# Optimization experiments

Measured on AMD Instinct MI355X. Metric: run time of the kernel, lower is better.

Reference implementation:

```python
import jax, jax.numpy as jnp
from jax import lax
import numpy as np

DN = ('NCHW', 'OIHW', 'NCHW')

def _conv(x, w, b, s):
    # torch Conv2d(kernel=3, padding=1, stride=s)
    y = lax.conv_general_dilated(x, w, (s, s), ((1, 1), (1, 1)), dimension_numbers=DN)
    return y + b[None, :, None, None]

def _convT(x, w, b, s):
    # torch ConvTranspose2d weight layout [in, out, kh, kw]; kernel=3, padding=1, output_padding=s-1
    wk = jnp.flip(w, (2, 3)).transpose(1, 0, 2, 3)  # -> OIHW
    y = lax.conv_general_dilated(x, wk, (1, 1), ((1, s), (1, s)), lhs_dilation=(s, s), dimension_numbers=DN)
    return y + b[None, :, None, None]

def _inorm(x, eps=1e-5):
    # torch InstanceNorm2d (affine=False)
    m = jnp.mean(x, (2, 3), keepdims=True)
    v = jnp.var(x, (2, 3), keepdims=True)
    return (x - m) * lax.rsqrt(v + eps)

def _prelu(x, a):
    return jnp.where(x >= 0, x, a * x)

def _block(x, w, b, a, s):
    return _prelu(_inorm(_conv(x, w, b, s)), a)

def _sage(x, src, tgt, wl, bl, wr, n):
    # PyG SAGEConv, mean aggregation: lin_l(scatter_mean(x[src] -> tgt)) + lin_r(x)
    deg = jnp.zeros((n,), x.dtype).at[tgt].add(1.0)
    agg = jnp.zeros((x.shape[0], n, x.shape[2]), x.dtype).at[:, tgt].add(x[:, src])
    agg = agg / jnp.maximum(deg, 1.0)[None, :, None]
    return jnp.einsum('bnc,oc->bno', agg, wl) + bl + jnp.einsum('bnc,oc->bno', x, wr)

def setup_inputs() -> dict:
    keys = iter(jax.random.split(jax.random.key(0), 64))
    def rn(shape, s=0.05):
        return jax.random.normal(next(keys), shape, jnp.float32) * s
    inp = {}
    inp['x'] = jax.random.normal(next(keys), (16, 1, 400, 400), jnp.float32)
    inp['edges'] = jax.random.randint(next(keys), (2, 5000), 0, 625, jnp.int32)
    for name, (ci, co) in zip(['d4', 'd3', 'd2', 'd1'], [(1, 32), (32, 64), (64, 128), (128, 256)]):
        inp['w_' + name] = rn((co, ci, 3, 3)); inp['b_' + name] = rn((co,))
        inp['a_' + name] = jnp.full((1,), 0.25, jnp.float32)
    inp['w_bot'] = rn((256, 256, 3, 3)); inp['b_bot'] = rn((256,))
    inp['a_bot'] = jnp.full((1,), 0.25, jnp.float32)
    for i in ['1', '2']:
        inp['wl' + i] = rn((256, 256)); inp['bl' + i] = rn((256,)); inp['wr' + i] = rn((256, 256))
    for name, (ci, co) in zip(['u1', 'u2', 'u3'], [(512, 128), (256, 64), (128, 32)]):
        inp['w_' + name] = rn((ci, co, 3, 3)); inp['b_' + name] = rn((co,))
        inp['a_' + name] = jnp.full((1,), 0.25, jnp.float32)
    inp['w_u4'] = rn((64, 2, 3, 3)); inp['b_u4'] = rn((2,))
    return inp

def reference(x, edges, w_d4, b_d4, a_d4, w_d3, b_d3, a_d3, w_d2, b_d2, a_d2, w_d1, b_d1, a_d1, w_bot, b_bot, a_bot, wl1, bl1, wr1, wl2, bl2, wr2, w_u1, b_u1, a_u1, w_u2, b_u2, a_u2, w_u3, b_u3, a_u3, w_u4, b_u4):
    xs = []
    x = _block(x, w_d4, b_d4, a_d4, 2); xs.append(x)   # [B,32,200,200]
    x = _block(x, w_d3, b_d3, a_d3, 2); xs.append(x)   # [B,64,100,100]
    x = _block(x, w_d2, b_d2, a_d2, 2); xs.append(x)   # [B,128,50,50]
    x = _block(x, w_d1, b_d1, a_d1, 2); xs.append(x)   # [B,256,25,25]
    x = _block(x, w_bot, b_bot, a_bot, 1)              # [B,256,25,25]
    B = x.shape[0]
    x = x.reshape(B, 256, -1).transpose(0, 2, 1)       # [B,625,256]
    src, tgt = edges[0], edges[1]
    x = jax.nn.relu(_sage(x, src, tgt, wl1, bl1, wr1, 625))
    x = jax.nn.relu(_sage(x, src, tgt, wl2, bl2, wr2, 625))
    x = x.transpose(0, 2, 1).reshape(B, 256, 25, 25)
    x = jnp.concatenate([xs[3], x], 1)                 # 512 ch
    x = _prelu(_inorm(_convT(x, w_u1, b_u1, 2)), a_u1) # [B,128,50,50]
    x = jnp.concatenate([xs[2], x], 1)
    x = _prelu(_inorm(_convT(x, w_u2, b_u2, 2)), a_u2) # [B,64,100,100]
    x = jnp.concatenate([xs[1], x], 1)
    x = _prelu(_inorm(_convT(x, w_u3, b_u3, 2)), a_u3) # [B,32,200,200]
    x = jnp.concatenate([xs[0], x], 1)
    return _convT(x, w_u4, b_u4, 2)                    # [B,2,400,400], conv_only top
```

## Files before the change

### kernel.cpp

```cpp
#include <hip/hip_runtime.h>
#include <hip/hip_bf16.h>

typedef __hip_bfloat16 bf16;

typedef __bf16 bf16x8 __attribute__((ext_vector_type(8)));
typedef float  f32x16 __attribute__((ext_vector_type(16)));

static __device__ __forceinline__ float bf(const bf16 v){ return __bfloat162float(v); }
static __device__ __forceinline__ float bfu(unsigned short u){
  unsigned fw = ((unsigned)u) << 16; float v; __builtin_memcpy(&v, &fw, 4); return v;
}

static __device__ __forceinline__ float ldm(const void* p, long i, int f){
  return f ? ((const float*)p)[i] : __bfloat162float(((const bf16*)p)[i]);
}
static __device__ __forceinline__ void stm(void* p, long i, int f, float v){
  if(f) ((float*)p)[i] = v; else ((bf16*)p)[i] = __float2bfloat16(v);
}
static __device__ __forceinline__ unsigned short bfbits(float v){
  __hip_bfloat16 h = __float2bfloat16(v);
  return *(unsigned short*)&h;
}

__global__ void k_detect(const void* __restrict__ w, int* __restrict__ mode){
  if(blockIdx.x == 0 && threadIdx.x == 0){
    const unsigned int* u = (const unsigned int*)w;
    int saneLo = 0;
    for(int i = 0; i < 64; i++){
      unsigned short lo = (unsigned short)(u[i] & 0xFFFFu);
      unsigned int fw = ((unsigned int)lo) << 16;
      float v; __builtin_memcpy(&v, &fw, 4);
      float a = fabsf(v);
      if(a > 1e-7f && a < 100.f) saneLo++;
    }
    *mode = (saneLo >= 48) ? 0 : 1;
  }
}

__global__ void k_wtrans(const void* __restrict__ w, float* __restrict__ wT,
                         const int* __restrict__ dmode, int C){
  int idx = blockIdx.x * 256 + threadIdx.x;
  if(idx >= C * C) return;
  int dm = *dmode;
  int o = idx % C, c = idx / C;
  wT[idx] = ldm(w, (long)o * C + c, dm);
}

__global__ void k_wtrans4(const void* __restrict__ w, bf16* __restrict__ wF,
                          const int* __restrict__ dmode, int Cin, int Cout){
  int idx = blockIdx.x * 256 + threadIdx.x;
  if(idx >= Cin * Cout * 9) return;
  int dm = *dmode;
  int e = idx & 7;
  int L = (idx >> 3) & 63;
  int r = idx >> 9;
  int NC = Cout >> 5;
  int nc = r % NC; r /= NC;
  int t  = r % 9;
  int kc = r / 9;
  int ci = kc*16 + (L>>5)*8 + e;
  int co = nc*32 + (L&31);
  wF[idx] = __float2bfloat16(ldm(w, ((long)ci*Cout + co)*9 + t, dm));
}

__global__ void k_wtrans5(const void* __restrict__ w, bf16* __restrict__ wF,
                          const int* __restrict__ dmode, int Cin, int Cout){
  int idx = blockIdx.x * 256 + threadIdx.x;
  if(idx >= Cin * Cout * 9) return;
  int dm = *dmode;
  int e = idx & 7;
  int L = (idx >> 3) & 63;
  int r = idx >> 9;
  int NC = Cout >> 5;
  int nc = r % NC; r /= NC;
  int t  = r % 9;
  int kc = r / 9;
  int ci = kc*16 + (L>>5)*8 + e;
  int co = nc*32 + (L&31);
  wF[idx] = __float2bfloat16(ldm(w, ((long)co*Cin + ci)*9 + t, dm));
}

__global__ __launch_bounds__(256, 4)
void k_conv_d4(const void* __restrict__ in, long in_off,
               const void* __restrict__ w, const void* __restrict__ bias,
               bf16* __restrict__ out, const int* __restrict__ dmode)
{
  __shared__ float sW[288];
  __shared__ float sB[32];
  int tid = threadIdx.x;
  int dm = *dmode;
  for(int e = tid; e < 288; e += 256) sW[e] = ldm(w, e, dm);
  if(tid < 32)  sB[tid] = ldm(bias, tid, dm);
  __syncthreads();
  int r = tid / 50, jt = tid % 50;
  if(r >= 5) return;
  int ho = blockIdx.x * 5 + r;
  int b  = blockIdx.z;
  int j0 = jt * 4;

  float x[3][9];
  long ibase = in_off + (long)b * 160000;
  #pragma unroll
  for(int rr = 0; rr < 3; rr++){
    int ir = 2*ho - 1 + rr;
    if(ir < 0 || ir >= 400){
      #pragma unroll
      for(int c = 0; c < 9; c++) x[rr][c] = 0.f;
      continue;
    }
    long rb = ibase + (long)ir * 400;
    int c0 = 2*j0 - 1;
    #pragma unroll
    for(int c = 0; c < 9; c++){
      int ic = c0 + c;
      x[rr][c] = (ic >= 0 && ic < 400) ? ldm(in, rb + ic, dm) : 0.f;
    }
  }

  long obase = ((long)b * 32) * 40000 + (long)ho * 200 + j0;
  for(int co = 0; co < 32; co++){
    const float* wv = &sW[co*9];
    float bv = sB[co];
    float a[4];
    #pragma unroll
    for(int p = 0; p < 4; p++){
      float s = bv;
      #pragma unroll
      for(int kh = 0; kh < 3; kh++)
        #pragma unroll
        for(int kw = 0; kw < 3; kw++)
          s += x[kh][2*p + kw] * wv[kh*3 + kw];
      a[p] = s;
    }
    ushort4 pk;
    pk.x = bfbits(a[0]); pk.y = bfbits(a[1]); pk.z = bfbits(a[2]); pk.w = bfbits(a[3]);
    *(ushort4*)&out[obase + (long)co * 40000] = pk;
  }
}

template<int CW, int NWC, int NWM, int S, int OCC>
__global__ __launch_bounds__(256, OCC)
void k_convSM(const void* __restrict__ in, long in_off, int fin_sel,
              const bf16* __restrict__ wF, const void* __restrict__ bias,
              void* __restrict__ out, int fout,
              const int* __restrict__ dmode,
              int Cin, int Hin, int Win, int Cout, int Hout, int Wout, int nym)
{
  constexpr int CP = 40;
  constexpr int HALF = CW/2;
  __shared__ unsigned short sX[3*CW*CP];
  int tid  = threadIdx.x;
  int lane = tid & 63;
  int wv   = tid >> 6;
  int nc   = wv % NWC;
  int mt   = wv / NWC;
  int ho   = blockIdx.x;
  int colg = blockIdx.y % nym;
  int cog  = blockIdx.y / nym;
  int b    = blockIdx.z;
  int dm   = *dmode;
  int fin  = (fin_sel == 2) ? dm : fin_sel;
  int NCtot = Cout >> 5;
  int chunk = cog*NWC + nc;
  int jl   = mt*32 + (lane & 31);
  int hi   = lane >> 5;
  int C0   = S*(colg*NWM*32);
  int ir0  = S*ho - 1;

  f32x16 acc;
  #pragma unroll
  for(int q = 0; q < 16; q++) acc[q] = 0.f;

  int p0, p1, p2;
  if(S == 2){ p0 = jl; p1 = HALF + jl; p2 = jl + 1; }
  else      { p0 = jl; p1 = jl + 1;    p2 = jl + 2; }

  for(int ci0 = 0; ci0 < Cin; ci0 += 32){
    for(int e = tid; e < 12*CW; e += 256){
      int c  = e % CW;
      int s  = e / CW;
      int kg = s & 3, r = s >> 2;
      int ir = ir0 + r;
      int ic = C0 - 1 + c;
      unsigned pk0, pk1, pk2, pk3;
      if(ir >= 0 && ir < Hin && ic >= 0 && ic < Win){
        long step = (long)Hin*Win;
        long base = in_off + ((long)b*Cin + ci0 + kg*8)*step + (long)ir*Win + ic;
        unsigned short t8[8];
        #pragma unroll
        for(int u = 0; u < 8; u++) t8[u] = bfbits(ldm(in, base + u*step, fin));
        pk0 = t8[0] | ((unsigned)t8[1]<<16);
        pk1 = t8[2] | ((unsigned)t8[3]<<16);
        pk2 = t8[4] | ((unsigned)t8[5]<<16);
        pk3 = t8[6] | ((unsigned)t8[7]<<16);
      } else { pk0=0; pk1=0; pk2=0; pk3=0; }
      int pos = (S == 2) ? ((c&1) ? HALF + (c>>1) : (c>>1)) : c;
      uint4 q; q.x=pk0; q.y=pk1; q.z=pk2; q.w=pk3;
      *(uint4*)&sX[(r*CW + pos)*CP + kg*8] = q;
    }
    __syncthreads();

    #pragma unroll
    for(int kg2 = 0; kg2 < 2; kg2++){
      int kbase = 8*hi + kg2*16;
      bf16x8 x[9];
      #pragma unroll
      for(int r = 0; r < 3; r++){
        x[r*3+0] = *(const bf16x8*)&sX[(r*CW + p0)*CP + kbase];
        x[r*3+1] = *(const bf16x8*)&sX[(r*CW + p1)*CP + kbase];
        x[r*3+2] = *(const bf16x8*)&sX[(r*CW + p2)*CP + kbase];
      }
      int kc = (ci0 >> 4) + kg2;
      const bf16x8* wb = ((const bf16x8*)wF) + ((long)(kc*9)*NCtot + chunk)*64 + lane;
      const long ws = (long)NCtot*64;
      #pragma unroll
      for(int t = 0; t < 9; t++){
        bf16x8 w = wb[(long)t*ws];
        acc = __builtin_amdgcn_mfma_f32_32x32x16_bf16(w, x[t], acc, 0,0,0);
      }
    }
    __syncthreads();
  }

  int j = colg*NWM*32 + jl;
  if(j < Wout){
    #pragma unroll
    for(int r16 = 0; r16 < 16; r16++){
      int co = chunk*32 + (r16&3) + 8*(r16>>2) + 4*hi;
      float bv = ldm(bias, co, dm);
      stm(out, ((long)b*Cout + co)*Hout*Wout + (long)ho*Wout + j, fout, acc[r16] + bv);
    }
  }
}

__global__ void k_inorm_prelu(void* __restrict__ x, int f, int HW,
                              const void* __restrict__ a, const int* __restrict__ dmode)
{
  int dm = *dmode;
  long base = (long)blockIdx.x * HW;
  float s = 0.f, s2 = 0.f;
  int vec = (f == 0) && ((HW & 3) == 0);
  if(vec){
    const ushort4* vp = (const ushort4*)((const bf16*)x + base);
    int n = HW >> 2;
    for(int i = threadIdx.x; i < n; i += 256){
      ushort4 v = vp[i];
      float a0 = bfu(v.x), a1 = bfu(v.y), a2 = bfu(v.z), a3 = bfu(v.w);
      s  += (a0 + a1) + (a2 + a3);
      s2 += (a0*a0 + a1*a1) + (a2*a2 + a3*a3);
    }
  } else {
    for(int i = threadIdx.x; i < HW; i += 256){ float v = ldm(x, base + i, f); s += v; s2 += v*v; }
  }
  __shared__ float sh[256], sh2[256];
  sh[threadIdx.x] = s; sh2[threadIdx.x] = s2; __syncthreads();
  for(int off = 128; off > 0; off >>= 1){
    if(threadIdx.x < off){ sh[threadIdx.x] += sh[threadIdx.x+off]; sh2[threadIdx.x] += sh2[threadIdx.x+off]; }
    __syncthreads();
  }
  float mean = sh[0] / HW;
  float var  = sh2[0] / HW - mean * mean;
  float inv  = rsqrtf(fmaxf(var, 0.f) + 1e-5f);
  float alpha = ldm(a, 0, dm);
  if(vec){
    ushort4* vp = (ushort4*)((bf16*)x + base);
    int n = HW >> 2;
    for(int i = threadIdx.x; i < n; i += 256){
      ushort4 v = vp[i];
      float t[4] = { bfu(v.x), bfu(v.y), bfu(v.z), bfu(v.w) };
      #pragma unroll
      for(int k = 0; k < 4; k++){
        float u = (t[k] - mean) * inv;
        t[k] = u >= 0.f ? u : alpha * u;
      }
      ushort4 o;
      o.x = bfbits(t[0]); o.y = bfbits(t[1]); o.z = bfbits(t[2]); o.w = bfbits(t[3]);
      vp[i] = o;
    }
  } else {
    for(int i = threadIdx.x; i < HW; i += 256){
      float v = (ldm(x, base + i, f) - mean) * inv;
      stm(x, base + i, f, v >= 0.f ? v : alpha * v);
    }
  }
}

__global__ void k_transpose(const float* __restrict__ in, float* __restrict__ out, int B, int C, int N){
  long idx = (long)blockIdx.x * 256 + threadIdx.x;
  long total = (long)B * C * N; if(idx >= total) return;
  int c = (int)(idx % C); long t = idx / C; int n = (int)(t % N); int b = (int)(t / N);
  out[idx] = in[((long)b * C + c) * N + n];
}

__global__ void k_deg(const int* __restrict__ tgt, float* __restrict__ deg, int E){
  int e = blockIdx.x * 256 + threadIdx.x;
  if(e < E) atomicAdd(&deg[tgt[e]], 1.0f);
}

__global__ void k_scatter(const float* __restrict__ xT, const int* __restrict__ src,
                          const int* __restrict__ tgt, float* __restrict__ agg,
                          int E, int C, int N, int B)
{
  int t = blockIdx.x * 256 + threadIdx.x;
  if(t >= E * C) return;
  int c = t % C; int e = t / C;
  int s = src[e], d = tgt[e];
  for(int b = 0; b < B; b++){
    atomicAdd(&agg[((long)b * N + d) * C + c], xT[((long)b * N + s) * C + c]);
  }
}

#define TN 5
__global__ void k_sage2(const float* __restrict__ xT, const float* __restrict__ agg,
                        const float* __restrict__ deg,
                        const float* __restrict__ wlT, const float* __restrict__ wrT,
                        const void* __restrict__ bl,
                        float* __restrict__ out, const int* __restrict__ dmode,
                        int B, int N, int C, int transpose_out)
{
  int o  = threadIdx.x;
  int n0 = blockIdx.x * TN;
  int b  = blockIdx.y;
  __shared__ float sX[TN][256];
  __shared__ float sA[TN][256];
  #pragma unroll
  for(int j = 0; j < TN; j++){
    int n = n0 + j;
    float dinv = 1.0f / fmaxf(deg[n], 1.0f);
    long base = ((long)b * N + n) * C;
    sX[j][o] = xT[base + o];
    sA[j][o] = agg[base + o] * dinv;
  }
  __syncthreads();
  int dm = *dmode;
  float bv = ldm(bl, o, dm);
  float acc[TN];
  #pragma unroll
  for(int j = 0; j < TN; j++) acc[j] = bv;
  #pragma unroll 4
  for(int c = 0; c < 256; c++){
    float wlv = wlT[(long)c * 256 + o];
    float wrv = wrT[(long)c * 256 + o];
    #pragma unroll
    for(int j = 0; j < TN; j++){
      acc[j] += sA[j][c] * wlv + sX[j][c] * wrv;
    }
  }
  #pragma unroll
  for(int j = 0; j < TN; j++){
    int n = n0 + j;
    float v = fmaxf(acc[j], 0.f);
    if(transpose_out) out[((long)b * C + o) * N + n] = v;
    else              out[((long)b * N + n) * C + o] = v;
  }
}

template<int CW, int NWC, int NWM, int OCC>
__global__ __launch_bounds__(256, OCC)
void k_convTM(const void* __restrict__ inA, int fA, int C1,
              const void* __restrict__ inB, int fB, int C2,
              const bf16* __restrict__ wF, const void* __restrict__ bias,
              bf16* __restrict__ out, const int* __restrict__ dmode,
              int Hin, int Win, int Cout)
{
  constexpr int CP = 40;
  __shared__ unsigned short sX[2*CW*CP];
  int tid  = threadIdx.x;
  int lane = tid & 63;
  int wv   = tid >> 6;
  int nc   = wv % NWC;
  int mt   = wv / NWC;
  int j0   = mt * 32;
  int i    = blockIdx.x;
  int b    = blockIdx.z;
  int dm   = *dmode;
  int Cin  = C1 + C2;
  int ln   = lane & 31;
  int hi   = lane >> 5;

  f32x16 acc0, acc1, acc2, acc3;
  #pragma unroll
  for(int q = 0; q < 16; q++){ acc0[q]=0.f; acc1[q]=0.f; acc2[q]=0.f; acc3[q]=0.f; }

  int xoff = (j0 + ln)*CP + 8*hi;

  for(int ci0 = 0; ci0 < Cin; ci0 += 32){
    for(int e = tid; e < 8*CW; e += 256){
      int col = e % CW;
      int s   = e / CW;
      int kg  = s & 3, row = s >> 2;
      int ii  = i + row;
      unsigned pk0, pk1, pk2, pk3;
      if(ii < Hin && col < Win){
        int cib = ci0 + kg*8;
        const void* sp; int ff; long base; long step = (long)Hin*Win;
        if(cib < C1){ sp = inA; ff = fA; base = ((long)b*C1 + cib)*step + (long)ii*Win + col; }
        else        { sp = inB; ff = fB; base = ((long)b*C2 + (cib-C1))*step + (long)ii*Win + col; }
        unsigned short t8[8];
        #pragma unroll
        for(int u = 0; u < 8; u++) t8[u] = bfbits(ldm(sp, base + u*step, ff));
        pk0 = t8[0] | ((unsigned)t8[1]<<16);
        pk1 = t8[2] | ((unsigned)t8[3]<<16);
        pk2 = t8[4] | ((unsigned)t8[5]<<16);
        pk3 = t8[6] | ((unsigned)t8[7]<<16);
      } else { pk0=0; pk1=0; pk2=0; pk3=0; }
      uint4 q; q.x=pk0; q.y=pk1; q.z=pk2; q.w=pk3;
      *(uint4*)&sX[(row*CW + col)*CP + kg*8] = q;
    }
    __syncthreads();

    #pragma unroll
    for(int kg2 = 0; kg2 < 2; kg2++){
      int base = xoff + kg2*16;
      bf16x8 x00 = *(const bf16x8*)&sX[base];
      bf16x8 x01 = *(const bf16x8*)&sX[base + CP];
      bf16x8 x10 = *(const bf16x8*)&sX[base + CW*CP];
      bf16x8 x11 = *(const bf16x8*)&sX[base + CW*CP + CP];
      int kc = (ci0 >> 4) + kg2;
      const bf16x8* wb = ((const bf16x8*)wF) + ((long)(kc*9)*NWC + nc)*64 + lane;
      const int ws = NWC*64;
      bf16x8 w0=wb[0],    w1=wb[ws],   w2=wb[2*ws], w3=wb[3*ws], w4=wb[4*ws],
             w5=wb[5*ws], w6=wb[6*ws], w7=wb[7*ws], w8=wb[8*ws];
      acc0 = __builtin_amdgcn_mfma_f32_32x32x16_bf16(w4, x00, acc0, 0,0,0);
      acc1 = __builtin_amdgcn_mfma_f32_32x32x16_bf16(w5, x00, acc1, 0,0,0);
      acc1 = __builtin_amdgcn_mfma_f32_32x32x16_bf16(w3, x01, acc1, 0,0,0);
      acc2 = __builtin_amdgcn_mfma_f32_32x32x16_bf16(w7, x00, acc2, 0,0,0);
      acc2 = __builtin_amdgcn_mfma_f32_32x32x16_bf16(w1, x10, acc2, 0,0,0);
      acc3 = __builtin_amdgcn_mfma_f32_32x32x16_bf16(w8, x00, acc3, 0,0,0);
      acc3 = __builtin_amdgcn_mfma_f32_32x32x16_bf16(w6, x01, acc3, 0,0,0);
      acc3 = __builtin_amdgcn_mfma_f32_32x32x16_bf16(w2, x10, acc3, 0,0,0);
      acc3 = __builtin_amdgcn_mfma_f32_32x32x16_bf16(w0, x11, acc3, 0,0,0);
    }
    __syncthreads();
  }

  int j = j0 + ln;
  if(j < Win){
    int Wout = 2*Win;
    #pragma unroll
    for(int r = 0; r < 16; r++){
      int co = nc*32 + (r&3) + 8*(r>>2) + 4*hi;
      float bv = ldm(bias, co, dm);
      long base0 = (((long)b*Cout + co)*2*Hin + 2*i)*(long)Wout + 2*j;
      unsigned p0 = bfbits(acc0[r]+bv) | ((unsigned)bfbits(acc1[r]+bv) << 16);
      unsigned p1 = bfbits(acc2[r]+bv) | ((unsigned)bfbits(acc3[r]+bv) << 16);
      *(unsigned*)&out[base0]        = p0;
      *(unsigned*)&out[base0 + Wout] = p1;
    }
  }
}

__global__ __launch_bounds__(256, 2)
void k_convT8(const bf16* __restrict__ inA, const bf16* __restrict__ inB,
              const void* __restrict__ w, const void* __restrict__ bias,
              void* __restrict__ out, long out_off, int fout_sel,
              const int* __restrict__ dmode, int Hin, int Win)
{
  __shared__ float sW[64*2*9];
  __shared__ float sB[2];
  int tid = threadIdx.x;
  int dm = *dmode;
  for(int e = tid; e < 64*2*9; e += 256) sW[e] = ldm(w, e, dm);
  if(tid < 2) sB[tid] = ldm(bias, tid, dm);
  __syncthreads();
  int r  = tid / 50;
  int jt = tid % 50;
  if(r >= 5) return;
  int i  = blockIdx.x * 5 + r;
  int b  = blockIdx.z;
  int j0 = jt * 4;
  int fout = (fout_sel == 2) ? dm : fout_sel;

  float acc[2][4][4];
  #pragma unroll
  for(int co = 0; co < 2; co++)
    #pragma unroll
    for(int p = 0; p < 4; p++){
      acc[co][p][0]=0.f; acc[co][p][1]=0.f; acc[co][p][2]=0.f; acc[co][p][3]=0.f;
    }

  bool e4   = (j0 + 4 < Win);
  bool row1 = (i + 1 < Hin);

  for(int ci = 0; ci < 64; ci++){
    const bf16* src = (ci < 32) ? inA : inB;
    int cc = ci & 31;
    const bf16* rp = src + ((long)b*32 + cc)*(long)Hin*Win + (long)i*Win + j0;
    float x0[5], x1[5];
    ushort4 v0 = *(const ushort4*)rp;
    x0[0]=bfu(v0.x); x0[1]=bfu(v0.y); x0[2]=bfu(v0.z); x0[3]=bfu(v0.w);
    x0[4] = e4 ? bf(rp[4]) : 0.f;
    if(row1){
      ushort4 v1 = *(const ushort4*)(rp + Win);
      x1[0]=bfu(v1.x); x1[1]=bfu(v1.y); x1[2]=bfu(v1.z); x1[3]=bfu(v1.w);
      x1[4] = e4 ? bf(rp[Win + 4]) : 0.f;
    } else {
      x1[0]=0.f; x1[1]=0.f; x1[2]=0.f; x1[3]=0.f; x1[4]=0.f;
    }
    const float* wp = &sW[ci*18];
    float wv[18];
    #pragma unroll
    for(int k = 0; k < 18; k++) wv[k] = wp[k];
    #pragma unroll
    for(int p = 0; p < 4; p++){
      float a00 = x0[p], a01 = x0[p+1], a10 = x1[p], a11 = x1[p+1];
      #pragma unroll
      for(int co = 0; co < 2; co++){
        const float* wc = &wv[co*9];
        acc[co][p][0] += a00*wc[4];
        acc[co][p][1] += a00*wc[5] + a01*wc[3];
        acc[co][p][2] += a00*wc[7] + a10*wc[1];
        acc[co][p][3] += a00*wc[8] + a01*wc[6] + a10*wc[2] + a11*wc[0];
      }
    }
  }
  int Wout = 2*Win;
  #pragma unroll
  for(int co = 0; co < 2; co++){
    float bv = sB[co];
    long base = out_off + (((long)b*2 + co)*2*Hin + 2*i)*(long)Wout + 2*j0;
    #pragma unroll
    for(int p = 0; p < 4; p++){
      stm(out, base + 2*p,            fout, acc[co][p][0] + bv);
      stm(out, base + 2*p + 1,        fout, acc[co][p][1] + bv);
      stm(out, base + 2*p + Wout,     fout, acc[co][p][2] + bv);
      stm(out, base + 2*p + Wout + 1, fout, acc[co][p][3] + bv);
    }
  }
}

static inline int cdiv(long a, long b){ return (int)((a + b - 1) / b); }

extern "C" void kernel_launch(void* const* d_in, const int* in_sizes, int n_in,
                              void* d_out, int out_size, void* d_ws, size_t ws_size,
                              hipStream_t stream) {
  const void* x_in  = d_in[0];
  const int*  edges = (const int*)d_in[1];
  const int* src = edges;
  const int* tgt = edges + 5000;
  const void *w_d4=d_in[2],  *b_d4=d_in[3],  *a_d4=d_in[4];
  const void *w_d3=d_in[5],  *b_d3=d_in[6],  *a_d3=d_in[7];
  const void *w_d2=d_in[8],  *b_d2=d_in[9],  *a_d2=d_in[10];
  const void *w_d1=d_in[11], *b_d1=d_in[12], *a_d1=d_in[13];
  const void *w_bot=d_in[14],*b_bot=d_in[15],*a_bot=d_in[16];
  const void *wl1=d_in[17], *bl1=d_in[18], *wr1=d_in[19];
  const void *wl2=d_in[20], *bl2=d_in[21], *wr2=d_in[22];
  const void *w_u1=d_in[23], *b_u1=d_in[24], *a_u1=d_in[25];
  const void *w_u2=d_in[26], *b_u2=d_in[27], *a_u2=d_in[28];
  const void *w_u3=d_in[29], *b_u3=d_in[30], *a_u3=d_in[31];
  const void *w_u4=d_in[32], *b_u4=d_in[33];

  const int NNODE = 625, E = 5000, CG = 256;

  const long TAIL = 4096 + 4*262144L + (589824L + 147456L + 36864L) * 2;
  const long ENCW = 976896L * 2;
  int Bc = 16;
  while(Bc > 1 && (7680000L * Bc + TAIL) > (long)ws_size) Bc >>= 1;
  int enc_in_pool = (Bc >= 8);
  if(!enc_in_pool){
    Bc = 16;
    while(Bc > 1 && (7680000L * Bc + TAIL + ENCW) > (long)ws_size) Bc >>= 1;
  }

  char* wsb = (char*)d_ws;
  long o_xs1  = 2560000L * Bc;
  long o_BIGA = 3840000L * Bc;
  long o_BIGB = 6400000L * Bc;
  long o_deg  = 7680000L * Bc;
  bf16*  xs0 = (bf16*)wsb;
  bf16*  xs1 = (bf16*)(wsb + o_xs1);
  bf16*  xs2 = (bf16*)(wsb + o_BIGA);
  bf16*  xs3 = (bf16*)(wsb + o_BIGA +  640000L*Bc);
  float* bot = (float*)(wsb + o_BIGA +  960000L*Bc);
  float* xT  = (float*)(wsb + o_BIGA + 1600000L*Bc);
  bf16*  u1  = (bf16*)(wsb + o_BIGA + 1600000L*Bc);
  bf16*  u3  = (bf16*)(wsb + o_BIGA);
  float* agg = (float*)(wsb + o_BIGB);
  float* g1  = (float*)(wsb + o_BIGB +  640000L*Bc);
  bf16*  u2  = (bf16*)(wsb + o_BIGB);
  float* deg = (float*)(wsb + o_deg);
  int*  mode = (int*)(wsb + o_deg + 3072);
  float* wlT1 = (float*)(wsb + o_deg + 4096);
  float* wrT1 = wlT1 + 65536;
  float* wlT2 = wrT1 + 65536;
  float* wrT2 = wlT2 + 65536;
  bf16*  wTu1 = (bf16*)(wrT2 + 65536);
  bf16*  wTu2 = wTu1 + 589824;
  bf16*  wTu3 = wTu2 + 147456;
  bf16*  wTd3 = enc_in_pool ? (bf16*)(wsb + o_BIGA + 2240000L*Bc) : (wTu3 + 36864);
  bf16*  wTd2 = wTd3 + 18432;
  bf16*  wTd1 = wTd2 + 73728;
  bf16*  wTdB = wTd1 + 294912;
  float* g2  = bot;

  hipLaunchKernelGGL(k_detect, dim3(1), dim3(1), 0, stream, w_d4, mode);

  hipMemsetAsync(deg, 0, NNODE*sizeof(float), stream);
  hipLaunchKernelGGL(k_deg, dim3(cdiv(E,256)), dim3(256), 0, stream, tgt, deg, E);
  hipLaunchKernelGGL(k_wtrans, dim3(256), dim3(256), 0, stream, wl1, wlT1, mode, CG);
  hipLaunchKernelGGL(k_wtrans, dim3(256), dim3(256), 0, stream, wr1, wrT1, mode, CG);
  hipLaunchKernelGGL(k_wtrans, dim3(256), dim3(256), 0, stream, wl2, wlT2, mode, CG);
  hipLaunchKernelGGL(k_wtrans, dim3(256), dim3(256), 0, stream, wr2, wrT2, mode, CG);
  hipLaunchKernelGGL(k_wtrans4, dim3(cdiv(589824,256)), dim3(256), 0, stream, w_u1, wTu1, mode, 512, 128);
  hipLaunchKernelGGL(k_wtrans4, dim3(cdiv(147456,256)), dim3(256), 0, stream, w_u2, wTu2, mode, 256, 64);
  hipLaunchKernelGGL(k_wtrans4, dim3(cdiv(36864,256)),  dim3(256), 0, stream, w_u3, wTu3, mode, 128, 32);

  for(int bo = 0; bo < 16; bo += Bc){
    long x_off   = (long)bo * 160000;
    long out_off = (long)bo * 320000;

    hipLaunchKernelGGL(k_wtrans5, dim3(cdiv(18432,256)),  dim3(256), 0, stream, w_d3, wTd3, mode, 32, 64);
    hipLaunchKernelGGL(k_wtrans5, dim3(cdiv(73728,256)),  dim3(256), 0, stream, w_d2, wTd2, mode, 64, 128);
    hipLaunchKernelGGL(k_wtrans5, dim3(cdiv(294912,256)), dim3(256), 0, stream, w_d1, wTd1, mode, 128, 256);
    hipLaunchKernelGGL(k_wtrans5, dim3(cdiv(589824,256)), dim3(256), 0, stream, w_bot, wTdB, mode, 256, 256);

    hipLaunchKernelGGL(k_conv_d4, dim3(40, 1, Bc), dim3(256), 0, stream,
                       x_in, x_off, w_d4, b_d4, xs0, mode);
    hipLaunchKernelGGL(k_inorm_prelu, dim3(Bc*32), dim3(256), 0, stream, xs0, 0, 40000, a_d4, mode);
    hipLaunchKernelGGL((k_convSM<130,2,2,2,4>), dim3(100, 2, Bc), dim3(256), 0, stream,
                       xs0, 0L, 0, wTd3, b_d3, xs1, 0, mode, 32, 200, 200, 64, 100, 100, 2);
    hipLaunchKernelGGL(k_inorm_prelu, dim3(Bc*64), dim3(256), 0, stream, xs1, 0, 10000, a_d3, mode);
    hipLaunchKernelGGL((k_convSM<66,4,1,2,4>), dim3(50, 2, Bc), dim3(256), 0, stream,
                       xs1, 0L, 0, wTd2, b_d2, xs2, 0, mode, 64, 100, 100, 128, 50, 50, 2);
    hipLaunchKernelGGL(k_inorm_prelu, dim3(Bc*128), dim3(256), 0, stream, xs2, 0, 2500, a_d2, mode);
    hipLaunchKernelGGL((k_convSM<66,4,1,2,4>), dim3(25, 2, Bc), dim3(256), 0, stream,
                       xs2, 0L, 0, wTd1, b_d1, xs3, 0, mode, 128, 50, 50, 256, 25, 25, 1);
    hipLaunchKernelGGL(k_inorm_prelu, dim3(Bc*256), dim3(256), 0, stream, xs3, 0, 625, a_d1, mode);
    hipLaunchKernelGGL((k_convSM<34,4,1,1,4>), dim3(25, 2, Bc), dim3(256), 0, stream,
                       xs3, 0L, 0, wTdB, b_bot, bot, 1, mode, 256, 25, 25, 256, 25, 25, 1);
    hipLaunchKernelGGL(k_inorm_prelu, dim3(Bc*256), dim3(256), 0, stream, bot, 1, 625, a_bot, mode);

    { long n = (long)Bc*CG*NNODE;
      hipLaunchKernelGGL(k_transpose, dim3(cdiv(n,256)), dim3(256), 0, stream, bot, xT, Bc, CG, NNODE); }
    hipMemsetAsync(agg, 0, 640000L*Bc, stream);
    hipLaunchKernelGGL(k_scatter, dim3(cdiv((long)E*CG,256)), dim3(256), 0, stream, xT, src, tgt, agg, E, CG, NNODE, Bc);
    hipLaunchKernelGGL(k_sage2, dim3(125, Bc), dim3(256), 0, stream,
                       xT, agg, deg, wlT1, wrT1, bl1, g1, mode, Bc, NNODE, CG, 0);
    hipMemsetAsync(agg, 0, 640000L*Bc, stream);
    hipLaunchKernelGGL(k_scatter, dim3(cdiv((long)E*CG,256)), dim3(256), 0, stream, g1, src, tgt, agg, E, CG, NNODE, Bc);
    hipLaunchKernelGGL(k_sage2, dim3(125, Bc), dim3(256), 0, stream,
                       g1, agg, deg, wlT2, wrT2, bl2, g2, mode, Bc, NNODE, CG, 1);

    hipLaunchKernelGGL((k_convTM<34,4,1,4>), dim3(25, 1, Bc), dim3(256), 0, stream,
                       xs3, 0, 256, g2, 1, 256, wTu1, b_u1, u1, mode, 25, 25, 128);
    hipLaunchKernelGGL(k_inorm_prelu, dim3(Bc*128), dim3(256), 0, stream, u1, 0, 2500, a_u1, mode);
    hipLaunchKernelGGL((k_convTM<66,2,2,4>), dim3(50, 1, Bc), dim3(256), 0, stream,
                       xs2, 0, 128, u1, 0, 128, wTu2, b_u2, u2, mode, 50, 50, 64);
    hipLaunchKernelGGL(k_inorm_prelu, dim3(Bc*64), dim3(256), 0, stream, u2, 0, 10000, a_u2, mode);
    hipLaunchKernelGGL((k_convTM<130,1,4,4>), dim3(100, 1, Bc), dim3(256), 0, stream,
                       xs1, 0, 64, u2, 0, 64, wTu3, b_u3, u3, mode, 100, 100, 32);
    hipLaunchKernelGGL(k_inorm_prelu, dim3(Bc*32), dim3(256), 0, stream, u3, 0, 40000, a_u3, mode);
    hipLaunchKernelGGL(k_convT8, dim3(40, 1, Bc), dim3(256), 0, stream,
                       xs0, u3, w_u4, b_u4, d_out, out_off, 2, mode, 200, 200);
  }
}
```

Measured before the change: 980.1 us.

## Run SAGE linear layers on bf16 MFMA with pre-swizzled weights

Replaces the scalar FP32 SAGE dense kernel with an MFMA 32x32x16 bf16 kernel. Node rows (x and degree-normalised aggregate) are staged to LDS as bf16, and the weights are pre-packed into the MFMA fragment layout by a new transpose kernel. The output is written either transposed or through an LDS-staged coalesced store. This cuts the FP32 FMA cost of the two 256x256 linear layers but lowers input and weight precision to bf16.

```diff
diff --git a/kernel.cpp b/kernel.cpp
--- a/kernel.cpp
+++ b/kernel.cpp
@@ -37,13 +37,19 @@
   }
 }
 
-__global__ void k_wtrans(const void* __restrict__ w, float* __restrict__ wT,
-                         const int* __restrict__ dmode, int C){
+__global__ void k_wtrans6(const void* __restrict__ w, bf16* __restrict__ wF,
+                          const int* __restrict__ dmode){
   int idx = blockIdx.x * 256 + threadIdx.x;
-  if(idx >= C * C) return;
+  if(idx >= 65536) return;
   int dm = *dmode;
-  int o = idx % C, c = idx / C;
-  wT[idx] = ldm(w, (long)o * C + c, dm);
+  int e = idx & 7;
+  int L = (idx >> 3) & 63;
+  int r = idx >> 9;
+  int nc = r & 7;
+  int kc = r >> 3;
+  int o = nc*32 + (L & 31);
+  int c = kc*16 + (L >> 5)*8 + e;
+  wF[idx] = __float2bfloat16(ldm(w, (long)o*256 + c, dm));
 }
 
 __global__ void k_wtrans4(const void* __restrict__ w, bf16* __restrict__ wF,
@@ -310,48 +316,89 @@
   }
 }
 
-#define TN 5
-__global__ void k_sage2(const float* __restrict__ xT, const float* __restrict__ agg,
-                        const float* __restrict__ deg,
-                        const float* __restrict__ wlT, const float* __restrict__ wrT,
-                        const void* __restrict__ bl,
-                        float* __restrict__ out, const int* __restrict__ dmode,
-                        int B, int N, int C, int transpose_out)
+__global__ __launch_bounds__(256, 4)
+void k_sageM(const float* __restrict__ xT, const float* __restrict__ agg,
+             const float* __restrict__ deg,
+             const bf16* __restrict__ wlF, const bf16* __restrict__ wrF,
+             const void* __restrict__ bl,
+             float* __restrict__ out, const int* __restrict__ dmode,
+             int NROW, int trans)
 {
-  int o  = threadIdx.x;
-  int n0 = blockIdx.x * TN;
-  int b  = blockIdx.y;
-  __shared__ float sX[TN][256];
-  __shared__ float sA[TN][256];
+  constexpr int CP = 264;
+  __shared__ unsigned short sS[2*32*CP];
+  int tid  = threadIdx.x;
+  int lane = tid & 63;
+  int wv   = tid >> 6;
+  int ln   = lane & 31;
+  int hi   = lane >> 5;
+  int n0   = blockIdx.x * 32;
+  int og0  = blockIdx.y * 128;
+  int ncg  = blockIdx.y*4 + wv;
+  int dm   = *dmode;
+
+  for(int e = tid; e < 4096; e += 256){
+    int c4 = e & 63;
+    int r  = (e >> 6) & 31;
+    int ar = e >> 11;
+    int row = n0 + r;
+    unsigned pk0 = 0, pk1 = 0;
+    if(row < NROW){
+      const float* sp = ar ? agg : xT;
+      float4 v = *(const float4*)&sp[(long)row*256 + c4*4];
+      if(ar){
+        int n = row % 625;
+        float dinv = 1.0f / fmaxf(deg[n], 1.0f);
+        v.x *= dinv; v.y *= dinv; v.z *= dinv; v.w *= dinv;
+      }
+      pk0 = bfbits(v.x) | ((unsigned)bfbits(v.y) << 16);
+      pk1 = bfbits(v.z) | ((unsigned)bfbits(v.w) << 16);
+    }
+    uint2 q; q.x = pk0; q.y = pk1;
+    *(uint2*)&sS[(ar*32 + r)*CP + c4*4] = q;
+  }
+  __syncthreads();
+
+  f32x16 acc;
   #pragma unroll
-  for(int j = 0; j < TN; j++){
-    int n = n0 + j;
-    float dinv = 1.0f / fmaxf(deg[n], 1.0f);
-    long base = ((long)b * N + n) * C;
-    sX[j][o] = xT[base + o];
-    sA[j][o] = agg[base + o] * dinv;
-  }
-  __syncthreads();
-  int dm = *dmode;
-  float bv = ldm(bl, o, dm);
-  float acc[TN];
+  for(int q = 0; q < 16; q++) acc[q] = 0.f;
+
+  int xb = ln*CP + 8*hi;
   #pragma unroll
-  for(int j = 0; j < TN; j++) acc[j] = bv;
-  #pragma unroll 4
-  for(int c = 0; c < 256; c++){
-    float wlv = wlT[(long)c * 256 + o];
-    float wrv = wrT[(long)c * 256 + o];
-    #pragma unroll
-    for(int j = 0; j < TN; j++){
-      acc[j] += sA[j][c] * wlv + sX[j][c] * wrv;
-    }
-  }
-  #pragma unroll
-  for(int j = 0; j < TN; j++){
-    int n = n0 + j;
-    float v = fmaxf(acc[j], 0.f);
-    if(transpose_out) out[((long)b * C + o) * N + n] = v;
-    else              out[((long)b * N + n) * C + o] = v;
+  for(int kc = 0; kc < 16; kc++){
+    bf16x8 bx = *(const bf16x8*)&sS[xb + kc*16];
+    bf16x8 ba = *(const bf16x8*)&sS[32*CP + xb + kc*16];
+    bf16x8 wl = ((const bf16x8*)wlF)[(long)(kc*8 + ncg)*64 + lane];
+    bf16x8 wr = ((const bf16x8*)wrF)[(long)(kc*8 + ncg)*64 + lane];
+    acc = __builtin_amdgcn_mfma_f32_32x32x16_bf16(wl, ba, acc, 0,0,0);
+    acc = __builtin_amdgcn_mfma_f32_32x32x16_bf16(wr, bx, acc, 0,0,0);
+  }
+
+  if(trans){
+    int row = n0 + ln;
+    if(row < NROW){
+      int b = row / 625, n = row - b*625;
+      #pragma unroll
+      for(int r16 = 0; r16 < 16; r16++){
+        int o = ncg*32 + (r16&3) + 8*(r16>>2) + 4*hi;
+        float v = acc[r16] + ldm(bl, o, dm);
+        out[((long)b*256 + o)*625 + n] = fmaxf(v, 0.f);
+      }
+    }
+  } else {
+    float* sO = (float*)sS;
+    __syncthreads();
+    #pragma unroll
+    for(int r16 = 0; r16 < 16; r16++){
+      int ol = wv*32 + (r16&3) + 8*(r16>>2) + 4*hi;
+      float v = acc[r16] + ldm(bl, og0 + ol, dm);
+      sO[ln*130 + ol] = fmaxf(v, 0.f);
+    }
+    __syncthreads();
+    for(int e = tid; e < 4096; e += 256){
+      int r = e >> 7, oc = e & 127;
+      int row = n0 + r;
+      if(row < NROW) out[(long)row*256 + og0 + oc] = sO[r*130 + oc];
+    }
   }
 }
 
@@ -580,11 +627,11 @@
   bf16*  u2  = (bf16*)(wsb + o_BIGB);
   float* deg = (float*)(wsb + o_deg);
   int*  mode = (int*)(wsb + o_deg + 3072);
-  float* wlT1 = (float*)(wsb + o_deg + 4096);
-  float* wrT1 = wlT1 + 65536;
-  float* wlT2 = wrT1 + 65536;
-  float* wrT2 = wlT2 + 65536;
-  bf16*  wTu1 = (bf16*)(wrT2 + 65536);
+  bf16*  wlF1 = (bf16*)(wsb + o_deg + 4096);
+  bf16*  wrF1 = wlF1 + 65536;
+  bf16*  wlF2 = wrF1 + 65536;
+  bf16*  wrF2 = wlF2 + 65536;
+  bf16*  wTu1 = (bf16*)(wsb + o_deg + 4096 + 4*262144L);
   bf16*  wTu2 = wTu1 + 589824;
   bf16*  wTu3 = wTu2 + 147456;
   bf16*  wTd3 = enc_in_pool ? (bf16*)(wsb + o_BIGA + 2240000L*Bc) : (wTu3 + 36864);
@@ -597,10 +644,10 @@
 
   hipMemsetAsync(deg, 0, NNODE*sizeof(float), stream);
   hipLaunchKernelGGL(k_deg, dim3(cdiv(E,256)), dim3(256), 0, stream, tgt, deg, E);
-  hipLaunchKernelGGL(k_wtrans, dim3(256), dim3(256), 0, stream, wl1, wlT1, mode, CG);
-  hipLaunchKernelGGL(k_wtrans, dim3(256), dim3(256), 0, stream, wr1, wrT1, mode, CG);
-  hipLaunchKernelGGL(k_wtrans, dim3(256), dim3(256), 0, stream, wl2, wlT2, mode, CG);
-  hipLaunchKernelGGL(k_wtrans, dim3(256), dim3(256), 0, stream, wr2, wrT2, mode, CG);
+  hipLaunchKernelGGL(k_wtrans6, dim3(256), dim3(256), 0, stream, wl1, wlF1, mode);
+  hipLaunchKernelGGL(k_wtrans6, dim3(256), dim3(256), 0, stream, wr1, wrF1, mode);
+  hipLaunchKernelGGL(k_wtrans6, dim3(256), dim3(256), 0, stream, wl2, wlF2, mode);
+  hipLaunchKernelGGL(k_wtrans6, dim3(256), dim3(256), 0, stream, wr2, wrF2, mode);
   hipLaunchKernelGGL(k_wtrans4, dim3(cdiv(589824,256)), dim3(256), 0, stream, w_u1, wTu1, mode, 512, 128);
   hipLaunchKernelGGL(k_wtrans4, dim3(cdiv(147456,256)), dim3(256), 0, stream, w_u2, wTu2, mode, 256, 64);
   hipLaunchKernelGGL(k_wtrans4, dim3(cdiv(36864,256)),  dim3(256), 0, stream, w_u3, wTu3, mode, 128, 32);
@@ -634,12 +681,12 @@
       hipLaunchKernelGGL(k_transpose, dim3(cdiv(n,256)), dim3(256), 0, stream, bot, xT, Bc, CG, NNODE); }
     hipMemsetAsync(agg, 0, 640000L*Bc, stream);
     hipLaunchKernelGGL(k_scatter, dim3(cdiv((long)E*CG,256)), dim3(256), 0, stream, xT, src, tgt, agg, E, CG, NNODE, Bc);
-    hipLaunchKernelGGL(k_sage2, dim3(125, Bc), dim3(256), 0, stream,
-                       xT, agg, deg, wlT1, wrT1, bl1, g1, mode, Bc, NNODE, CG, 0);
+    hipLaunchKernelGGL(k_sageM, dim3(cdiv((long)Bc*NNODE,32), 2), dim3(256), 0, stream,
+                       xT, agg, deg, wlF1, wrF1, bl1, g1, mode, Bc*NNODE, 0);
     hipMemsetAsync(agg, 0, 640000L*Bc, stream);
     hipLaunchKernelGGL(k_scatter, dim3(cdiv((long)E*CG,256)), dim3(256), 0, stream, g1, src, tgt, agg, E, CG, NNODE, Bc);
-    hipLaunchKernelGGL(k_sage2, dim3(125, Bc), dim3(256), 0, stream,
-                       g1, agg, deg, wlT2, wrT2, bl2, g2, mode, Bc, NNODE, CG, 1);
+    hipLaunchKernelGGL(k_sageM, dim3(cdiv((long)Bc*NNODE,32), 2), dim3(256), 0, stream,
+                       g1, agg, deg, wlF2, wrF2, bl2, g2, mode, Bc*NNODE, 1);
 
     hipLaunchKernelGGL((k_convTM<34,4,1,4>), dim3(25, 1, Bc), dim3(256), 0, stream,
                        xs3, 0, 256, g2, 1, 256, wTu1, b_u1, u1, mode, 25, 25, 128);
```

New measurement: 884.6 us. 1.11x faster.
